# Performance work log

Measured on AMD Instinct MI355X. Metric: run time of the kernel, lower is better.

Reference implementation:

```python
import jax, jax.numpy as jnp
import numpy as np

INF = 1000000.0
BG = 1000000
NUM_CLASS = 80
IMG = 1024
B = 8
G = 50
STRIDES = (8, 16, 32, 64, 128)
RANGES = ((-1.0, 64.0), (64.0, 128.0), (128.0, 256.0), (256.0, 512.0), (512.0, INF))


def _meshgrids():
    pts, rngs = [], []
    for s, (lo, hi) in zip(STRIDES, RANGES):
        n = IMG // s
        c = (jnp.arange(n, dtype=jnp.float32) + 0.5) * s
        yy, xx = jnp.meshgrid(c, c, indexing='ij')  # row-major over (h, w)
        pts.append(jnp.stack([xx.ravel(), yy.ravel()], axis=-1))  # [n*n, 2] (x, y)
        rngs.append(jnp.tile(jnp.array([lo, hi], jnp.float32), (n * n, 1)))
    return pts, rngs


def setup_inputs() -> dict:
    key = jax.random.key(0)
    k1, k2, k3, k4, k5, k6 = jax.random.split(key, 6)
    M = sum((IMG // s) ** 2 for s in STRIDES)  # 21824
    T = B * M
    pred_class = jax.random.normal(k1, (T, NUM_CLASS), dtype=jnp.float32)
    pred_bbox = jax.random.uniform(k2, (T, 4), dtype=jnp.float32) * 256.0  # raw ltrb distances
    pred_centerness = jax.random.normal(k3, (T,), dtype=jnp.float32)
    xy1 = jax.random.uniform(k4, (B, G, 2), dtype=jnp.float32) * (IMG - 64)
    wh = jax.random.uniform(k5, (B, G, 2), dtype=jnp.float32) * 256.0 + 8.0
    gt_boxes = jnp.concatenate([xy1, jnp.clip(xy1 + wh, 0.0, float(IMG))], axis=-1)
    gt_labels = jax.random.randint(k6, (B, G), 1, NUM_CLASS + 1, dtype=jnp.int32)  # 1-indexed
    return {'pred_class': pred_class, 'pred_bbox': pred_bbox,
            'pred_centerness': pred_centerness, 'gt_boxes': gt_boxes, 'gt_labels': gt_labels}


def _fcos_losses(pred_class, pred_bbox, pred_centerness, gt_boxes, gt_labels):
    mesh_l, rng_l = _meshgrids()
    mesh = jnp.concatenate(mesh_l, axis=0)        # [M, 2]
    ranges = jnp.concatenate(rng_l, axis=0)       # [M, 2]
    ns = [m.shape[0] for m in mesh_l]
    offs = np.concatenate([[0], np.cumsum(ns)])

    def assign(boxes, labels):  # boxes [G,4], labels [G]
        l = mesh[:, None, 0] - boxes[None, :, 0]
        t = mesh[:, None, 1] - boxes[None, :, 1]
        r = boxes[None, :, 2] - mesh[:, None, 0]
        b = boxes[None, :, 3] - mesh[:, None, 1]
        ltrb = jnp.stack([l, t, r, b], axis=-1)   # [M, G, 4]
        inside = ltrb.min(axis=-1) > 0
        mx = ltrb.max(axis=-1)
        in_rng = (mx >= ranges[:, None, 0]) & (mx <= ranges[:, None, 1])
        areas = (boxes[:, 2] - boxes[:, 0]) * (boxes[:, 3] - boxes[:, 1])
        masked = jnp.where(inside & in_rng, areas[None, :], INF)
        idx = jnp.argmin(masked, axis=1)
        min_area = jnp.take_along_axis(masked, idx[:, None], axis=1)[:, 0]
        lab = jnp.where(min_area >= INF, BG, labels[idx])
        bt = jnp.take_along_axis(ltrb, idx[:, None, None], axis=1)[:, 0]
        return lab, bt

    labels_t, bbox_t = jax.vmap(assign)(gt_boxes, gt_labels)  # [B, M], [B, M, 4]

    # reorder to level-major then batch-major (matches permute_and_flatten + per-level cat)
    nl = len(ns)
    class_targets = jnp.concatenate([labels_t[:, offs[i]:offs[i + 1]].reshape(-1) for i in range(nl)])
    bbox_targets = jnp.concatenate([bbox_t[:, offs[i]:offs[i + 1]].reshape(-1, 4) for i in range(nl)])
    flat_mesh = jnp.concatenate([jnp.tile(mesh_l[i], (B, 1)) for i in range(nl)])

    pos = class_targets != BG
    posf = pos.astype(pred_class.dtype)
    pos_num = jnp.maximum(posf.sum(), 1.0)

    # one-hot (bg rows all zero); labels are 1-indexed
    onehot = jax.nn.one_hot(jnp.where(pos, class_targets - 1, NUM_CLASS), NUM_CLASS, dtype=pred_class.dtype)

    # sigmoid focal loss (gamma=2, alpha=0.25), averaged by pos_num
    p = jax.nn.sigmoid(pred_class)
    ce = -(onehot * jax.nn.log_sigmoid(pred_class) + (1.0 - onehot) * jax.nn.log_sigmoid(-pred_class))
    pt = p * onehot + (1.0 - p) * (1.0 - onehot)
    w = (0.25 * onehot + 0.75 * (1.0 - onehot)) * (1.0 - pt) ** 2
    loss_cls = jnp.sum(w * ce) / pos_num

    # centerness target sqrt((min_lr/max_lr)*(min_tb/max_tb))
    l, t, r, b = bbox_targets[:, 0], bbox_targets[:, 1], bbox_targets[:, 2], bbox_targets[:, 3]
    num = jnp.minimum(l, r) * jnp.minimum(t, b)
    den = jnp.maximum(l, r) * jnp.maximum(t, b) + 1e-12
    ctr = jnp.where(pos, jnp.sqrt(jnp.clip(num / den, 0.0, 1.0)), 0.0)

    # decode both pred and target distances to xyxy boxes (distance2bbox)
    def d2b(d):
        return jnp.stack([flat_mesh[:, 0] - d[:, 0], flat_mesh[:, 1] - d[:, 1],
                          flat_mesh[:, 0] + d[:, 2], flat_mesh[:, 1] + d[:, 3]], axis=-1)

    pb, tb = d2b(pred_bbox), d2b(bbox_targets)

    # IoU loss = -log(iou), weighted by centerness targets, normalized by their sum
    ix1 = jnp.maximum(pb[:, 0], tb[:, 0]); iy1 = jnp.maximum(pb[:, 1], tb[:, 1])
    ix2 = jnp.minimum(pb[:, 2], tb[:, 2]); iy2 = jnp.minimum(pb[:, 3], tb[:, 3])
    inter = jnp.clip(ix2 - ix1, 0.0) * jnp.clip(iy2 - iy1, 0.0)
    ap = jnp.clip(pb[:, 2] - pb[:, 0], 0.0) * jnp.clip(pb[:, 3] - pb[:, 1], 0.0)
    at = jnp.clip(tb[:, 2] - tb[:, 0], 0.0) * jnp.clip(tb[:, 3] - tb[:, 1], 0.0)
    iou = inter / (ap + at - inter + 1e-7)
    denorm = jnp.maximum(jnp.sum(ctr), 1e-6)
    loss_box = jnp.sum(-jnp.log(jnp.clip(iou, 1e-6, 1.0)) * ctr) / denorm

    # centerness BCE-with-logits, mean over positives
    bce = -(ctr * jax.nn.log_sigmoid(pred_centerness) + (1.0 - ctr) * jax.nn.log_sigmoid(-pred_centerness))
    loss_ctr = jnp.sum(bce * posf) / pos_num

    return jnp.stack([loss_cls, loss_box, loss_ctr])


def reference(pred_class, pred_bbox, pred_centerness, gt_boxes, gt_labels):
    return _fcos_losses(pred_class, pred_bbox, pred_centerness, gt_boxes, gt_labels)
```

## Files before the change

kernel.cpp:

```cpp
#include <hip/hip_runtime.h>

typedef float f32x4 __attribute__((ext_vector_type(4)));

#define TPB 256
#define ABLK 682
#define SBLK 1364
#define GRID 2046
#define TPB_F 1024
#define GNUM 50
#define INF_ 1000000.0f
#define L2E  1.44269504088896f
#define C_STREAM 0.519860385f

__device__ __forceinline__ void sp_parts(float xx, float& s2, float& apl, float& bb) {
    float a  = fabsf(xx);
    float e  = __expf(-a);
    float t  = 1.0f + e;
    float r  = __builtin_amdgcn_rcpf(t);
    float ln = __logf(t);
    s2  = r * r;
    apl = a + ln;
    bb  = e * e * ln;
}

__device__ __forceinline__ float stream_elem(float x, float acc) {
    float t = __builtin_amdgcn_exp2f(x * L2E);
    float u = 1.0f + t;
    float p = t * __builtin_amdgcn_rcpf(u);
    float lg = __builtin_amdgcn_logf(u);
    return fmaf(p * p, lg, acc);
}

__global__ __launch_bounds__(TPB) void fcos_fat(
    const float* __restrict__ pred_class,
    const float4* __restrict__ pred_bbox,
    const float* __restrict__ pred_ctr,
    const float4* __restrict__ gt_boxes,
    const int* __restrict__ gt_labels,
    float* __restrict__ partials)
{
    const int tid = threadIdx.x;
    const int bid = blockIdx.x;
    const int lane = tid & 63, wid = tid >> 6;

    if (bid >= ABLK) {
        __shared__ float wsum[4];
        const int s = bid - ABLK;
        const f32x4* pc4 = (const f32x4*)pred_class + (size_t)s * 2560;
        f32x4 v[10];
        #pragma unroll
        for (int it = 0; it < 10; ++it) v[it] = pc4[tid + it * TPB];

        float a0 = 0.f, a1 = 0.f, a2 = 0.f, a3 = 0.f;
        #pragma unroll
        for (int it = 0; it < 10; ++it) {
            a0 = stream_elem(v[it].x, a0);
            a1 = stream_elem(v[it].y, a1);
            a2 = stream_elem(v[it].z, a2);
            a3 = stream_elem(v[it].w, a3);
        }
        float acc = (a0 + a1) + (a2 + a3);
        #pragma unroll
        for (int off = 32; off >= 1; off >>= 1) acc += __shfl_down(acc, off);
        if (lane == 0) wsum[wid] = acc;
        __syncthreads();
        if (tid == 0)
            partials[5 * ABLK + s] = (wsum[0] + wsum[1]) + (wsum[2] + wsum[3]);
    } else {
        __shared__ float wpart[4][5];
        const int a = bid;
        const int k = (a << 8) + tid;

        float4 dpred = pred_bbox[k];
        float  pcv   = pred_ctr[k];

        int li, b, p;
        if (k < 131072)      { li = 0; b = k >> 14;               p = k & 16383; }
        else if (k < 163840) { li = 1; int t = k - 131072; b = t >> 12; p = t & 4095; }
        else if (k < 172032) { li = 2; int t = k - 163840; b = t >> 10; p = t & 1023; }
        else if (k < 174080) { li = 3; int t = k - 172032; b = t >> 8;  p = t & 255; }
        else                 { li = 4; int t = k - 174080; b = t >> 6;  p = t & 63; }

        const int logn = 7 - li;
        const float sF = (float)(8 << li);
        const float x = ((float)(p & ((1 << logn) - 1)) + 0.5f) * sF;
        const float y = ((float)(p >> logn) + 0.5f) * sF;
        const float lo = (li == 0) ? -1.0f : (float)(64 << (li - 1));
        const float hi = (li == 4) ? INF_ : (float)(64 << li);

        const float4* gb = gt_boxes + b * GNUM;
        float best = INF_;
        int bi = 0;
        #pragma unroll 5
        for (int g = 0; g < GNUM; ++g) {
            float4 bx = gb[g];
            float l  = x - bx.x;
            float t  = y - bx.y;
            float rr = bx.z - x;
            float bt = bx.w - y;
            float mn = fminf(fminf(l, t), fminf(rr, bt));
            float mx = fmaxf(fmaxf(l, t), fmaxf(rr, bt));
            float area = (bx.z - bx.x) * (bx.w - bx.y);
            bool ok = (mn > 0.0f) && (mx >= lo) && (mx <= hi);
            float m = ok ? area : INF_;
            if (m < best) { best = m; bi = g; }
        }

        const bool pos = best < INF_;
        float ctr = 0.0f, lbox = 0.0f, bce = 0.0f, posf = 0.0f, cls = 0.0f;
        if (pos) {
            posf = 1.0f;
            int lab = gt_labels[b * GNUM + bi] - 1;
            float xx = pred_class[(size_t)k * 80 + lab];
            float4 bx = gb[bi];
            float wl = x - bx.x, wt = y - bx.y, wr = bx.z - x, wb = bx.w - y;

            float num = fminf(wl, wr) * fminf(wt, wb);
            float den = fmaxf(wl, wr) * fmaxf(wt, wb) + 1e-12f;
            ctr = __builtin_amdgcn_sqrtf(
                      fminf(fmaxf(num * __builtin_amdgcn_rcpf(den), 0.0f), 1.0f));

            float px1 = x - dpred.x, py1 = y - dpred.y, px2 = x + dpred.z, py2 = y + dpred.w;
            float tx1 = x - wl,  ty1 = y - wt,  tx2 = x + wr,  ty2 = y + wb;
            float ix1 = fmaxf(px1, tx1), iy1 = fmaxf(py1, ty1);
            float ix2 = fminf(px2, tx2), iy2 = fminf(py2, ty2);
            float inter = fmaxf(ix2 - ix1, 0.0f) * fmaxf(iy2 - iy1, 0.0f);
            float ap = fmaxf(px2 - px1, 0.0f) * fmaxf(py2 - py1, 0.0f);
            float at = fmaxf(tx2 - tx1, 0.0f) * fmaxf(ty2 - ty1, 0.0f);
            float iou = inter * __builtin_amdgcn_rcpf(ap + at - inter + 1e-7f);
            lbox = -__logf(fminf(fmaxf(iou, 1e-6f), 1.0f)) * ctr;

            float e  = __expf(-fabsf(pcv));
            float l1 = __logf(1.0f + e);
            float sp_p = fmaxf(pcv, 0.0f) + l1;
            float sp_n = fmaxf(-pcv, 0.0f) + l1;
            bce = ctr * sp_n + (1.0f - ctr) * sp_p;

            float s2c, aplc, bbc;
            sp_parts(xx, s2c, aplc, bbc);
            float nt = (xx >= 0.0f) ? aplc : bbc;
            float tg = (xx >= 0.0f) ? bbc : aplc;
            cls = s2c * fmaf(0.25f, tg, -0.75f * nt);
        }

        float v5[5] = {cls, lbox, bce, posf, ctr};
        #pragma unroll
        for (int off = 32; off >= 1; off >>= 1) {
            #pragma unroll
            for (int s2 = 0; s2 < 5; ++s2) v5[s2] += __shfl_down(v5[s2], off);
        }
        if (lane == 0) {
            #pragma unroll
            for (int s2 = 0; s2 < 5; ++s2) wpart[wid][s2] = v5[s2];
        }
        __syncthreads();
        if (tid == 0) {
            #pragma unroll
            for (int s2 = 0; s2 < 5; ++s2)
                partials[s2 * ABLK + a] =
                    (wpart[0][s2] + wpart[1][s2]) + (wpart[2][s2] + wpart[3][s2]);
        }
    }
}

__global__ __launch_bounds__(TPB_F) void fcos_final(
    const float* __restrict__ partials, float* __restrict__ out)
{
    const int tid = threadIdx.x;
    float acc[5] = {0, 0, 0, 0, 0};
    float accs = 0.0f;
    for (int i = tid; i < ABLK; i += TPB_F) {
        #pragma unroll
        for (int s2 = 0; s2 < 5; ++s2) acc[s2] += partials[s2 * ABLK + i];
    }
    for (int i = tid; i < SBLK; i += TPB_F) accs += partials[5 * ABLK + i];
    #pragma unroll
    for (int off = 32; off >= 1; off >>= 1) {
        #pragma unroll
        for (int s2 = 0; s2 < 5; ++s2) acc[s2] += __shfl_down(acc[s2], off);
        accs += __shfl_down(accs, off);
    }
    __shared__ float wp[16][6];
    const int lane = tid & 63, wid = tid >> 6;
    if (lane == 0) {
        #pragma unroll
        for (int s2 = 0; s2 < 5; ++s2) wp[wid][s2] = acc[s2];
        wp[wid][5] = accs;
    }
    __syncthreads();
    if (tid == 0) {
        float S[6];
        #pragma unroll
        for (int s2 = 0; s2 < 6; ++s2) {
            float s = 0.0f;
            #pragma unroll
            for (int w = 0; w < 16; ++w) s += wp[w][s2];
            S[s2] = s;
        }
        float pos_num = fmaxf(S[3], 1.0f);
        float denorm  = fmaxf(S[4], 1e-6f);
        out[0] = fmaf(C_STREAM, S[5], S[0]) / pos_num;
        out[1] = S[1] / denorm;
        out[2] = S[2] / pos_num;
    }
}

extern "C" void kernel_launch(void* const* d_in, const int* in_sizes, int n_in,
                              void* d_out, int out_size, void* d_ws, size_t ws_size,
                              hipStream_t stream) {
    const float*  pred_class = (const float*)d_in[0];
    const float4* pred_bbox  = (const float4*)d_in[1];
    const float*  pred_ctr   = (const float*)d_in[2];
    const float4* gt_boxes   = (const float4*)d_in[3];
    const int*    gt_labels  = (const int*)d_in[4];
    float* partials = (float*)d_ws;
    float* out = (float*)d_out;

    fcos_fat<<<GRID, TPB, 0, stream>>>(pred_class, pred_bbox, pred_ctr,
                                       gt_boxes, gt_labels, partials);
    fcos_final<<<1, TPB_F, 0, stream>>>(partials, out);
}
```

Before: 22.45 us.

## Fuse stream and assignment blocks; split GT scan across thread pairs

Replaces the heterogeneous grid, where some blocks streamed the class logits and others did per-point GT assignment, with one uniform kernel. Each block now loads its logit slice, then does the assignment for 128 points. Each point's 50-box scan is split across two adjacent threads and merged with a lane shuffle that breaks ties by lowest index. The aim is to overlap the logit-load latency with assignment math and to shorten the serial GT loop. The cost is higher register pressure from holding the loaded vectors across the assignment work, and half the threads sit idle during the positive-sample math.

```diff
diff --git a/kernel.cpp b/kernel.cpp
--- a/kernel.cpp
+++ b/kernel.cpp
@@ -3,9 +3,8 @@
 typedef float f32x4 __attribute__((ext_vector_type(4)));
 
 #define TPB 256
-#define ABLK 682
-#define SBLK 1364
-#define GRID 2046
+#define PPB 128
+#define NBLK 1364
 #define TPB_F 1024
 #define GNUM 50
 #define INF_ 1000000.0f
@@ -31,7 +30,7 @@
     return fmaf(p * p, lg, acc);
 }
 
-__global__ __launch_bounds__(TPB) void fcos_fat(
+__global__ __launch_bounds__(TPB, 2) void fcos_fused(
     const float* __restrict__ pred_class,
     const float4* __restrict__ pred_bbox,
     const float* __restrict__ pred_ctr,
@@ -39,127 +38,123 @@
     const int* __restrict__ gt_labels,
     float* __restrict__ partials)
 {
+    __shared__ float wpart[4][5];
+
     const int tid = threadIdx.x;
-    const int bid = blockIdx.x;
+    const int sub = tid & 1;
+    const int pt  = tid >> 1;
+    const int k   = (blockIdx.x << 7) + pt;
+
+    const f32x4* pc4 = (const f32x4*)pred_class + (size_t)blockIdx.x * 2560;
+    f32x4 v[10];
+    #pragma unroll
+    for (int it = 0; it < 10; ++it) v[it] = pc4[tid + it * TPB];
+
+    float4 dpred = pred_bbox[k];
+    float  pcv   = pred_ctr[k];
+
+    int li, b, p;
+    if (k < 131072)      { li = 0; b = k >> 14;               p = k & 16383; }
+    else if (k < 163840) { li = 1; int t = k - 131072; b = t >> 12; p = t & 4095; }
+    else if (k < 172032) { li = 2; int t = k - 163840; b = t >> 10; p = t & 1023; }
+    else if (k < 174080) { li = 3; int t = k - 172032; b = t >> 8;  p = t & 255; }
+    else                 { li = 4; int t = k - 174080; b = t >> 6;  p = t & 63; }
+
+    const int logn = 7 - li;
+    const float sF = (float)(8 << li);
+    const float x = ((float)(p & ((1 << logn) - 1)) + 0.5f) * sF;
+    const float y = ((float)(p >> logn) + 0.5f) * sF;
+    const float lo = (li == 0) ? -1.0f : (float)(64 << (li - 1));
+    const float hi = (li == 4) ? INF_ : (float)(64 << li);
+
+    const float4* gb = gt_boxes + b * GNUM;
+    float best = INF_;
+    int bi = GNUM;
+    #pragma unroll 5
+    for (int j = 0; j < 25; ++j) {
+        int g = sub * 25 + j;
+        float4 bx = gb[g];
+        float l  = x - bx.x;
+        float t  = y - bx.y;
+        float rr = bx.z - x;
+        float bt = bx.w - y;
+        float mn = fminf(fminf(l, t), fminf(rr, bt));
+        float mx = fmaxf(fmaxf(l, t), fmaxf(rr, bt));
+        float area = (bx.z - bx.x) * (bx.w - bx.y);
+        bool ok = (mn > 0.0f) && (mx >= lo) && (mx <= hi);
+        float m = ok ? area : INF_;
+        if (m < best) { best = m; bi = g; }
+    }
+    {
+        float ob = __shfl_xor(best, 1);
+        int   oi = __shfl_xor(bi, 1);
+        if (ob < best || (ob == best && oi < bi)) { best = ob; bi = oi; }
+    }
+
+    const bool pos = best < INF_;
+    float ctr = 0.0f, lbox = 0.0f, bce = 0.0f, posf = 0.0f, cls = 0.0f;
+    if (sub == 0 && pos) {
+        posf = 1.0f;
+        int lab = gt_labels[b * GNUM + bi] - 1;
+        float xx = pred_class[(size_t)k * 80 + lab];
+        float4 bx = gb[bi];
+        float wl = x - bx.x, wt = y - bx.y, wr = bx.z - x, wb = bx.w - y;
+
+        float num = fminf(wl, wr) * fminf(wt, wb);
+        float den = fmaxf(wl, wr) * fmaxf(wt, wb) + 1e-12f;
+        ctr = __builtin_amdgcn_sqrtf(
+                  fminf(fmaxf(num * __builtin_amdgcn_rcpf(den), 0.0f), 1.0f));
+
+        float px1 = x - dpred.x, py1 = y - dpred.y, px2 = x + dpred.z, py2 = y + dpred.w;
+        float tx1 = x - wl,  ty1 = y - wt,  tx2 = x + wr,  ty2 = y + wb;
+        float ix1 = fmaxf(px1, tx1), iy1 = fmaxf(py1, ty1);
+        float ix2 = fminf(px2, tx2), iy2 = fminf(py2, ty2);
+        float inter = fmaxf(ix2 - ix1, 0.0f) * fmaxf(iy2 - iy1, 0.0f);
+        float ap = fmaxf(px2 - px1, 0.0f) * fmaxf(py2 - py1, 0.0f);
+        float at = fmaxf(tx2 - tx1, 0.0f) * fmaxf(ty2 - ty1, 0.0f);
+        float iou = inter * __builtin_amdgcn_rcpf(ap + at - inter + 1e-7f);
+        lbox = -__logf(fminf(fmaxf(iou, 1e-6f), 1.0f)) * ctr;
+
+        float e  = __expf(-fabsf(pcv));
+        float l1 = __logf(1.0f + e);
+        float sp_p = fmaxf(pcv, 0.0f) + l1;
+        float sp_n = fmaxf(-pcv, 0.0f) + l1;
+        bce = ctr * sp_n + (1.0f - ctr) * sp_p;
+
+        float s2c, aplc, bbc;
+        sp_parts(xx, s2c, aplc, bbc);
+        float nt = (xx >= 0.0f) ? aplc : bbc;
+        float tg = (xx >= 0.0f) ? bbc : aplc;
+        cls = s2c * fmaf(0.25f, tg, -0.75f * nt);
+    }
+
+    float a0 = 0.f, a1 = 0.f, a2 = 0.f, a3 = 0.f;
+    #pragma unroll
+    for (int it = 0; it < 10; ++it) {
+        a0 = stream_elem(v[it].x, a0);
+        a1 = stream_elem(v[it].y, a1);
+        a2 = stream_elem(v[it].z, a2);
+        a3 = stream_elem(v[it].w, a3);
+    }
+    cls = fmaf(C_STREAM, (a0 + a1) + (a2 + a3), cls);
+
+    float v5[5] = {cls, lbox, bce, posf, ctr};
+    #pragma unroll
+    for (int off = 32; off >= 1; off >>= 1) {
+        #pragma unroll
+        for (int s2 = 0; s2 < 5; ++s2) v5[s2] += __shfl_down(v5[s2], off);
+    }
     const int lane = tid & 63, wid = tid >> 6;
-
-    if (bid >= ABLK) {
-        __shared__ float wsum[4];
-        const int s = bid - ABLK;
-        const f32x4* pc4 = (const f32x4*)pred_class + (size_t)s * 2560;
-        f32x4 v[10];
-        #pragma unroll
-        for (int it = 0; it < 10; ++it) v[it] = pc4[tid + it * TPB];
-
-        float a0 = 0.f, a1 = 0.f, a2 = 0.f, a3 = 0.f;
-        #pragma unroll
-        for (int it = 0; it < 10; ++it) {
-            a0 = stream_elem(v[it].x, a0);
-            a1 = stream_elem(v[it].y, a1);
-            a2 = stream_elem(v[it].z, a2);
-            a3 = stream_elem(v[it].w, a3);
-        }
-        float acc = (a0 + a1) + (a2 + a3);
-        #pragma unroll
-        for (int off = 32; off >= 1; off >>= 1) acc += __shfl_down(acc, off);
-        if (lane == 0) wsum[wid] = acc;
-        __syncthreads();
-        if (tid == 0)
-            partials[5 * ABLK + s] = (wsum[0] + wsum[1]) + (wsum[2] + wsum[3]);
-    } else {
-        __shared__ float wpart[4][5];
-        const int a = bid;
-        const int k = (a << 8) + tid;
-
-        float4 dpred = pred_bbox[k];
-        float  pcv   = pred_ctr[k];
-
-        int li, b, p;
-        if (k < 131072)      { li = 0; b = k >> 14;               p = k & 16383; }
-        else if (k < 163840) { li = 1; int t = k - 131072; b = t >> 12; p = t & 4095; }
-        else if (k < 172032) { li = 2; int t = k - 163840; b = t >> 10; p = t & 1023; }
-        else if (k < 174080) { li = 3; int t = k - 172032; b = t >> 8;  p = t & 255; }
-        else                 { li = 4; int t = k - 174080; b = t >> 6;  p = t & 63; }
-
-        const int logn = 7 - li;
-        const float sF = (float)(8 << li);
-        const float x = ((float)(p & ((1 << logn) - 1)) + 0.5f) * sF;
-        const float y = ((float)(p >> logn) + 0.5f) * sF;
-        const float lo = (li == 0) ? -1.0f : (float)(64 << (li - 1));
-        const float hi = (li == 4) ? INF_ : (float)(64 << li);
-
-        const float4* gb = gt_boxes + b * GNUM;
-        float best = INF_;
-        int bi = 0;
-        #pragma unroll 5
-        for (int g = 0; g < GNUM; ++g) {
-            float4 bx = gb[g];
-            float l  = x - bx.x;
-            float t  = y - bx.y;
-            float rr = bx.z - x;
-            float bt = bx.w - y;
-            float mn = fminf(fminf(l, t), fminf(rr, bt));
-            float mx = fmaxf(fmaxf(l, t), fmaxf(rr, bt));
-            float area = (bx.z - bx.x) * (bx.w - bx.y);
-            bool ok = (mn > 0.0f) && (mx >= lo) && (mx <= hi);
-            float m = ok ? area : INF_;
-            if (m < best) { best = m; bi = g; }
-        }
-
-        const bool pos = best < INF_;
-        float ctr = 0.0f, lbox = 0.0f, bce = 0.0f, posf = 0.0f, cls = 0.0f;
-        if (pos) {
-            posf = 1.0f;
-            int lab = gt_labels[b * GNUM + bi] - 1;
-            float xx = pred_class[(size_t)k * 80 + lab];
-            float4 bx = gb[bi];
-            float wl = x - bx.x, wt = y - bx.y, wr = bx.z - x, wb = bx.w - y;
-
-            float num = fminf(wl, wr) * fminf(wt, wb);
-            float den = fmaxf(wl, wr) * fmaxf(wt, wb) + 1e-12f;
-            ctr = __builtin_amdgcn_sqrtf(
-                      fminf(fmaxf(num * __builtin_amdgcn_rcpf(den), 0.0f), 1.0f));
-
-            float px1 = x - dpred.x, py1 = y - dpred.y, px2 = x + dpred.z, py2 = y + dpred.w;
-            float tx1 = x - wl,  ty1 = y - wt,  tx2 = x + wr,  ty2 = y + wb;
-            float ix1 = fmaxf(px1, tx1), iy1 = fmaxf(py1, ty1);
-            float ix2 = fminf(px2, tx2), iy2 = fminf(py2, ty2);
-            float inter = fmaxf(ix2 - ix1, 0.0f) * fmaxf(iy2 - iy1, 0.0f);
-            float ap = fmaxf(px2 - px1, 0.0f) * fmaxf(py2 - py1, 0.0f);
-            float at = fmaxf(tx2 - tx1, 0.0f) * fmaxf(ty2 - ty1, 0.0f);
-            float iou = inter * __builtin_amdgcn_rcpf(ap + at - inter + 1e-7f);
-            lbox = -__logf(fminf(fmaxf(iou, 1e-6f), 1.0f)) * ctr;
-
-            float e  = __expf(-fabsf(pcv));
-            float l1 = __logf(1.0f + e);
-            float sp_p = fmaxf(pcv, 0.0f) + l1;
-            float sp_n = fmaxf(-pcv, 0.0f) + l1;
-            bce = ctr * sp_n + (1.0f - ctr) * sp_p;
-
-            float s2c, aplc, bbc;
-            sp_parts(xx, s2c, aplc, bbc);
-            float nt = (xx >= 0.0f) ? aplc : bbc;
-            float tg = (xx >= 0.0f) ? bbc : aplc;
-            cls = s2c * fmaf(0.25f, tg, -0.75f * nt);
-        }
-
-        float v5[5] = {cls, lbox, bce, posf, ctr};
-        #pragma unroll
-        for (int off = 32; off >= 1; off >>= 1) {
-            #pragma unroll
-            for (int s2 = 0; s2 < 5; ++s2) v5[s2] += __shfl_down(v5[s2], off);
-        }
-        if (lane == 0) {
-            #pragma unroll
-            for (int s2 = 0; s2 < 5; ++s2) wpart[wid][s2] = v5[s2];
-        }
-        __syncthreads();
-        if (tid == 0) {
-            #pragma unroll
-            for (int s2 = 0; s2 < 5; ++s2)
-                partials[s2 * ABLK + a] =
-                    (wpart[0][s2] + wpart[1][s2]) + (wpart[2][s2] + wpart[3][s2]);
-        }
+    if (lane == 0) {
+        #pragma unroll
+        for (int s2 = 0; s2 < 5; ++s2) wpart[wid][s2] = v5[s2];
+    }
+    __syncthreads();
+    if (tid == 0) {
+        #pragma unroll
+        for (int s2 = 0; s2 < 5; ++s2)
+            partials[s2 * NBLK + blockIdx.x] =
+                (wpart[0][s2] + wpart[1][s2]) + (wpart[2][s2] + wpart[3][s2]);
     }
 }
 
@@ -168,30 +163,26 @@
 {
     const int tid = threadIdx.x;
     float acc[5] = {0, 0, 0, 0, 0};
-    float accs = 0.0f;
-    for (int i = tid; i < ABLK; i += TPB_F) {
-        #pragma unroll
-        for (int s2 = 0; s2 < 5; ++s2) acc[s2] += partials[s2 * ABLK + i];
-    }
-    for (int i = tid; i < SBLK; i += TPB_F) accs += partials[5 * ABLK + i];
+    for (int i = tid; i < NBLK; i += TPB_F) {
+        #pragma unroll
+        for (int s2 = 0; s2 < 5; ++s2) acc[s2] += partials[s2 * NBLK + i];
+    }
     #pragma unroll
     for (int off = 32; off >= 1; off >>= 1) {
         #pragma unroll
         for (int s2 = 0; s2 < 5; ++s2) acc[s2] += __shfl_down(acc[s2], off);
-        accs += __shfl_down(accs, off);
-    }
-    __shared__ float wp[16][6];
+    }
+    __shared__ float wp[16][5];
     const int lane = tid & 63, wid = tid >> 6;
     if (lane == 0) {
         #pragma unroll
         for (int s2 = 0; s2 < 5; ++s2) wp[wid][s2] = acc[s2];
-        wp[wid][5] = accs;
     }
     __syncthreads();
     if (tid == 0) {
-        float S[6];
-        #pragma unroll
-        for (int s2 = 0; s2 < 6; ++s2) {
+        float S[5];
+        #pragma unroll
+        for (int s2 = 0; s2 < 5; ++s2) {
             float s = 0.0f;
             #pragma unroll
             for (int w = 0; w < 16; ++w) s += wp[w][s2];
@@ -199,7 +190,7 @@
         }
         float pos_num = fmaxf(S[3], 1.0f);
         float denorm  = fmaxf(S[4], 1e-6f);
-        out[0] = fmaf(C_STREAM, S[5], S[0]) / pos_num;
+        out[0] = S[0] / pos_num;
         out[1] = S[1] / denorm;
         out[2] = S[2] / pos_num;
     }
@@ -216,7 +207,7 @@
     float* partials = (float*)d_ws;
     float* out = (float*)d_out;
 
-    fcos_fat<<<GRID, TPB, 0, stream>>>(pred_class, pred_bbox, pred_ctr,
-                                       gt_boxes, gt_labels, partials);
+    fcos_fused<<<NBLK, TPB, 0, stream>>>(pred_class, pred_bbox, pred_ctr,
+                                         gt_boxes, gt_labels, partials);
     fcos_final<<<1, TPB_F, 0, stream>>>(partials, out);
 }
```

After: 25.78 us. 14.8% more time.
